# Kernel optimization log

Hardware: AMD Instinct MI355X
Metric: run time of the kernel (lower is better)

The kernel has to match this reference:

```python
import jax, jax.numpy as jnp
import numpy as np

B, N, H = 1024, 100, 256
CLIP = 10.0


def setup_inputs() -> dict:
    key = jax.random.key(0)
    ks = jax.random.split(key, 14)
    s = 0.05  # param scale for numerical stability
    return {
        "x": jax.random.uniform(ks[0], (B, N, 2), jnp.float32),
        "encoder_output": jax.random.normal(ks[1], (B, N, H), jnp.float32),
        "W_ih1": jax.random.normal(ks[2], (3 * H, H + 1), jnp.float32) * s,
        "W_hh1": jax.random.normal(ks[3], (3 * H, H), jnp.float32) * s,
        "b_ih1": jax.random.normal(ks[4], (3 * H,), jnp.float32) * s,
        "b_hh1": jax.random.normal(ks[5], (3 * H,), jnp.float32) * s,
        "W_ih2": jax.random.normal(ks[6], (3 * H, H), jnp.float32) * s,
        "W_hh2": jax.random.normal(ks[7], (3 * H, H), jnp.float32) * s,
        "b_ih2": jax.random.normal(ks[8], (3 * H,), jnp.float32) * s,
        "b_hh2": jax.random.normal(ks[9], (3 * H,), jnp.float32) * s,
        "W_q": jax.random.normal(ks[10], (H, H), jnp.float32) * s,
        "W_ref": jax.random.normal(ks[11], (H, H), jnp.float32) * s,
        "v": jax.random.normal(ks[12], (H,), jnp.float32) * s,
    }


def gru_cell(x, h, W_ih, W_hh, b_ih, b_hh):
    # Standard torch GRU cell math (gate order r, z, n).
    gi = x @ W_ih.T + b_ih
    gh = h @ W_hh.T + b_hh
    i_r, i_z, i_n = jnp.split(gi, 3, axis=-1)
    h_r, h_z, h_n = jnp.split(gh, 3, axis=-1)
    r = jax.nn.sigmoid(i_r + h_r)
    z = jax.nn.sigmoid(i_z + h_z)
    n = jnp.tanh(i_n + r * h_n)
    return (1.0 - z) * n + z * h


def reference(x, encoder_output, W_ih1, W_hh1, b_ih1, b_hh1,
              W_ih2, W_hh2, b_ih2, b_hh2, W_q, W_ref, v):
    Bs, Nn, Hh = encoder_output.shape
    dt = encoder_output.dtype
    # Pointer reference projection is step-invariant -> hoist out of the loop.
    ref = jnp.einsum('bnh,hk->bnk', encoder_output, W_ref)  # [B,N,H]
    bidx = jnp.arange(Bs)
    mask0 = jnp.zeros((Bs, Nn), bool)
    # t=1 context: graph embedding + full remaining capacity D=1.
    ctx0 = jnp.concatenate([encoder_output.mean(1), jnp.ones((Bs, 1), dt)], -1)
    D0 = jnp.ones((Bs,), dt)

    def step(carry, _):
        mask, ctx, D = carry
        z0 = jnp.zeros((Bs, Hh), dt)
        # torch code calls self.gru(last_x) with fresh zero hidden every step
        h1 = gru_cell(ctx, z0, W_ih1, W_hh1, b_ih1, b_hh1)
        h2 = gru_cell(h1, z0, W_ih2, W_hh2, b_ih2, b_hh2)
        q = h2 @ W_q  # [B,H]
        u = CLIP * jnp.tanh(jnp.einsum('bnh,h->bn', jnp.tanh(q[:, None, :] + ref), v))
        u = jnp.where(mask, -1e9, u)  # masked_fill_(mask, -inf)
        nxt = jnp.argmax(u, axis=-1)  # greedy decode (deterministic baseline)
        logp = jax.nn.log_softmax(u, axis=-1)[bidx, nxt]
        mask = mask | (jnp.arange(Nn)[None, :] == nxt[:, None])
        D = D - 1.0 / Nn
        ctx = jnp.concatenate([encoder_output[bidx, nxt], D[:, None]], -1)
        return (mask, ctx, D), (nxt, logp)

    _, (pi_t, lps) = jax.lax.scan(step, (mask0, ctx0, D0), None, length=Nn)
    pi = pi_t.T  # [B, N] tour
    ll = lps.sum(0)  # [B] log-likelihood of tour
    coords = x[bidx[:, None], pi]  # [B,N,2]
    nxt_coords = jnp.roll(coords, -1, axis=1)
    cost = jnp.sqrt(((coords - nxt_coords) ** 2).sum(-1)).sum(-1)  # closed tour length
    return cost, ll
```

## Files before the change

kernel.cpp:

```cpp
#include <hip/hip_runtime.h>
#include <cstdint>
#include <cmath>

#define BATCH 1024
#define SEQ   100
#define HD    256
#define HD3   768
#define NTHR  512
#define NSRC  101

__device__ __forceinline__ float sigmoidf_(float x) { return 1.0f / (1.0f + expf(-x)); }

__device__ __forceinline__ float gru0(float gr, float gz, float gn, float hr, float hz, float hn) {
    float r = sigmoidf_(gr + hr);
    float z = sigmoidf_(gz + hz);
    float n = tanhf(gn + r * hn);
    return (1.0f - z) * n;
}

__global__ __launch_bounds__(256) void init_mean_kernel(const float* __restrict__ enc,
                                                        float* __restrict__ meanenc) {
    int b = blockIdx.x, tid = threadIdx.x;
    const float* e = enc + (size_t)b * SEQ * HD + tid;
    float s = 0.f;
    for (int n = 0; n < SEQ; ++n) s += e[(size_t)n * HD];
    meanenc[(size_t)b * HD + tid] = s * (1.0f / SEQ);
}

__global__ __launch_bounds__(256) void prep_kernel(const float* __restrict__ W_ih1,
                                                   const float* __restrict__ W_ih2,
                                                   float4* __restrict__ W1p4,
                                                   float4* __restrict__ W2p4,
                                                   float* __restrict__ wl,
                                                   float* __restrict__ biasz) {
    int k = blockIdx.x, t = threadIdx.x;
    W1p4[k * HD + t] = make_float4(W_ih1[(size_t)t * (HD + 1) + k],
                                   W_ih1[(size_t)(t + HD) * (HD + 1) + k],
                                   W_ih1[(size_t)(t + 2 * HD) * (HD + 1) + k], 0.f);
    W2p4[k * HD + t] = make_float4(W_ih2[(size_t)t * HD + k],
                                   W_ih2[(size_t)(t + HD) * HD + k],
                                   W_ih2[(size_t)(t + 2 * HD) * HD + k], 0.f);
    if (k == 0) {
#pragma unroll
        for (int c = 0; c < 3; ++c) wl[c * HD + t] = W_ih1[(size_t)(c * HD + t) * (HD + 1) + HD];
        biasz[t] = 0.f;
    }
}

__global__ __launch_bounds__(256) void gemm_bias_kernel(const float* __restrict__ A, int lda,
                                                        const float* __restrict__ Bm, int ldb,
                                                        const float* __restrict__ bias,
                                                        float* __restrict__ C, int ldc) {
    __shared__ float As[16][68];
    __shared__ float Bs[16][68];
    const int tid = threadIdx.x;
    const int tx = tid & 15, ty = tid >> 4;
    const int mBase = blockIdx.x * 64, nBase = blockIdx.y * 64;
    const int lr = tid >> 2, lc = (tid & 3) << 2;
    const int bkk = tid >> 4, bn4 = (tid & 15) << 2;
    float acc[4][4] = {};
    for (int k0 = 0; k0 < HD; k0 += 16) {
        float4 av = *(const float4*)&A[(size_t)(mBase + lr) * lda + k0 + lc];
        As[lc + 0][lr] = av.x; As[lc + 1][lr] = av.y; As[lc + 2][lr] = av.z; As[lc + 3][lr] = av.w;
        float4 bv = *(const float4*)&Bm[(size_t)(k0 + bkk) * ldb + nBase + bn4];
        *(float4*)&Bs[bkk][bn4] = bv;
        __syncthreads();
#pragma unroll
        for (int kk = 0; kk < 16; ++kk) {
            const float4 a4 = *(const float4*)&As[kk][ty << 2];
            const float4 b4 = *(const float4*)&Bs[kk][tx << 2];
            const float ar_[4] = {a4.x, a4.y, a4.z, a4.w};
            const float br_[4] = {b4.x, b4.y, b4.z, b4.w};
#pragma unroll
            for (int i = 0; i < 4; ++i)
#pragma unroll
                for (int j = 0; j < 4; ++j) acc[i][j] = fmaf(ar_[i], br_[j], acc[i][j]);
        }
        __syncthreads();
    }
#pragma unroll
    for (int i = 0; i < 4; ++i) {
        float o[4];
#pragma unroll
        for (int j = 0; j < 4; ++j) o[j] = acc[i][j] + bias[nBase + (tx << 2) + j];
        *(float4*)&C[(size_t)(mBase + (ty << 2) + i) * ldc + nBase + (tx << 2)] =
            make_float4(o[0], o[1], o[2], o[3]);
    }
}

__global__ __launch_bounds__(512) void g1_kernel(const float* __restrict__ enc,
                                                 const float* __restrict__ meanenc,
                                                 const float4* __restrict__ W1p4,
                                                 float* __restrict__ G1) {
    __shared__ float srcs[16][HD];
    __shared__ float part[16][3][HD];
    const int b = blockIdx.x, tid = threadIdx.x;
    const int col = tid & 255, kh = tid >> 8;
    const int kb = kh << 7;
    const float4* wpc = W1p4 + ((size_t)kb << 8) + col;

    for (int nb = 0; nb < 112; nb += 16) {
        for (int e = tid; e < 16 * 64; e += NTHR) {
            const int r = e >> 6, f = e & 63;
            const int n = nb + r;
            float4 vsrc = make_float4(0.f, 0.f, 0.f, 0.f);
            if (n < SEQ)
                vsrc = *(const float4*)&enc[((size_t)b * SEQ + n) * HD + (f << 2)];
            else if (n == SEQ)
                vsrc = *(const float4*)&meanenc[(size_t)b * HD + (f << 2)];
            *(float4*)&srcs[r][f << 2] = vsrc;
        }
        __syncthreads();

        float acc[16][3] = {};
        for (int k = 0; k < 128; k += 8) {
            float4 wv[8];
#pragma unroll
            for (int u = 0; u < 8; ++u) wv[u] = wpc[(size_t)(k + u) << 8];
#pragma unroll
            for (int n = 0; n < 16; ++n) {
#pragma unroll
                for (int uu = 0; uu < 2; ++uu) {
                    const float4 h = *(const float4*)&srcs[n][kb + k + (uu << 2)];
                    const float hv[4] = {h.x, h.y, h.z, h.w};
#pragma unroll
                    for (int u = 0; u < 4; ++u) {
                        const float4 w4 = wv[(uu << 2) + u];
                        acc[n][0] = fmaf(hv[u], w4.x, acc[n][0]);
                        acc[n][1] = fmaf(hv[u], w4.y, acc[n][1]);
                        acc[n][2] = fmaf(hv[u], w4.z, acc[n][2]);
                    }
                }
            }
        }

        if (kh) {
#pragma unroll
            for (int n = 0; n < 16; ++n)
#pragma unroll
                for (int g = 0; g < 3; ++g) part[n][g][col] = acc[n][g];
        }
        __syncthreads();
        if (!kh) {
#pragma unroll
            for (int n = 0; n < 16; ++n) {
                const int nn = nb + n;
                if (nn < NSRC) {
                    float* gp = G1 + ((size_t)(b * NSRC + nn)) * HD3 + col;
                    gp[0]       = acc[n][0] + part[n][0][col];
                    gp[HD]      = acc[n][1] + part[n][1][col];
                    gp[2 * HD]  = acc[n][2] + part[n][2][col];
                }
            }
        }
        __syncthreads();
    }
}

__global__ __launch_bounds__(512, 2) void decode_g1(const float* __restrict__ refb,
                                                    const float* __restrict__ G1,
                                                    const float4* __restrict__ W2p4,
                                                    const float* __restrict__ W_q,
                                                    const float* __restrict__ b_ih1,
                                                    const float* __restrict__ b_hh1,
                                                    const float* __restrict__ b_ih2,
                                                    const float* __restrict__ b_hh2,
                                                    const float* __restrict__ wl,
                                                    const float* __restrict__ vvec,
                                                    const float* __restrict__ x,
                                                    float* __restrict__ out) {
    __shared__ float wls[HD3], bi1s[HD3], bhh1s[HD3], bi2s[HD3], bhh2s[HD3];
    __shared__ float vs[HD];
    __shared__ float h1s[4][HD];
    __shared__ float h2s[4][HD];
    __shared__ float qs[4][HD];
    __shared__ float part[4][3][HD];
    __shared__ float us[4][SEQ];
    __shared__ int   mask_s[4][SEQ];
    __shared__ int   pi_s[4][SEQ];
    __shared__ float ll_s[4];

    const int blk = blockIdx.x, tid = threadIdx.x;
    const int w = tid >> 6, lane = tid & 63;
    const int col = tid & 255, kh = tid >> 8;
    const int b0 = blk << 2;

    for (int j = tid; j < HD3; j += NTHR) {
        wls[j] = wl[j];
        bi1s[j] = b_ih1[j];
        bhh1s[j] = b_hh1[j];
        bi2s[j] = b_ih2[j];
        bhh2s[j] = b_hh2[j];
    }
    if (tid < HD) vs[tid] = vvec[tid];
    if (tid < SEQ) {
#pragma unroll
        for (int bb = 0; bb < 4; ++bb) mask_s[bb][tid] = 0;
    }
    if (tid < 4) ll_s[tid] = 0.f;
    __syncthreads();

    for (int e = tid; e < 4 * HD; e += NTHR) {
        const int bb = e >> 8, c = e & 255;
        const float* gp = G1 + ((size_t)((b0 + bb) * NSRC + SEQ)) * HD3;
        float gr = gp[c] + bi1s[c];                 gr += 1.0f * wls[c];
        float gz = gp[HD + c] + bi1s[c + HD];       gz += 1.0f * wls[c + HD];
        float gn = gp[2 * HD + c] + bi1s[c + 2 * HD]; gn += 1.0f * wls[c + 2 * HD];
        h1s[bb][c] = gru0(gr, gz, gn, bhh1s[c], bhh1s[c + HD], bhh1s[c + 2 * HD]);
    }
    __syncthreads();

    float Dreg = 1.0f;
    const float invN = 1.0f / SEQ;

    auto gru2_phase = [&]() {
        float acc[4][3] = {};
        const int kb = kh << 7;
        const float4* wpc = W2p4 + ((size_t)kb << 8) + col;
        for (int k = 0; k < 128; k += 16) {
            float4 wv[16];
#pragma unroll
            for (int u = 0; u < 16; ++u) wv[u] = wpc[(size_t)(k + u) << 8];
#pragma unroll
            for (int uu = 0; uu < 4; ++uu) {
#pragma unroll
                for (int bb = 0; bb < 4; ++bb) {
                    const float4 h = *(const float4*)&h1s[bb][kb + k + (uu << 2)];
                    const float hv[4] = {h.x, h.y, h.z, h.w};
#pragma unroll
                    for (int u = 0; u < 4; ++u) {
                        const float4 w4 = wv[(uu << 2) + u];
                        acc[bb][0] = fmaf(hv[u], w4.x, acc[bb][0]);
                        acc[bb][1] = fmaf(hv[u], w4.y, acc[bb][1]);
                        acc[bb][2] = fmaf(hv[u], w4.z, acc[bb][2]);
                    }
                }
            }
        }
        if (kh) {
#pragma unroll
            for (int bb = 0; bb < 4; ++bb)
#pragma unroll
                for (int g = 0; g < 3; ++g) part[bb][g][col] = acc[bb][g];
        }
        __syncthreads();
        if (!kh) {
#pragma unroll
            for (int bb = 0; bb < 4; ++bb) {
                float gr = acc[bb][0] + part[bb][0][col] + bi2s[col];
                float gz = acc[bb][1] + part[bb][1][col] + bi2s[col + HD];
                float gn = acc[bb][2] + part[bb][2][col] + bi2s[col + 2 * HD];
                h2s[bb][col] = gru0(gr, gz, gn, bhh2s[col], bhh2s[col + HD], bhh2s[col + 2 * HD]);
            }
        }
    };

    for (int t = 0; t < SEQ; ++t) {
        gru2_phase();
        __syncthreads();
        {
            float qa[4] = {};
            const int kb = kh << 7;
            const float* wqc = W_q + ((size_t)kb << 8) + col;
            for (int k = 0; k < 128; k += 16) {
                float wv[16];
#pragma unroll
                for (int u = 0; u < 16; ++u) wv[u] = wqc[(size_t)(k + u) << 8];
#pragma unroll
                for (int uu = 0; uu < 4; ++uu) {
#pragma unroll
                    for (int bb = 0; bb < 4; ++bb) {
                        const float4 h = *(const float4*)&h2s[bb][kb + k + (uu << 2)];
                        qa[bb] = fmaf(h.x, wv[(uu << 2) + 0], qa[bb]);
                        qa[bb] = fmaf(h.y, wv[(uu << 2) + 1], qa[bb]);
                        qa[bb] = fmaf(h.z, wv[(uu << 2) + 2], qa[bb]);
                        qa[bb] = fmaf(h.w, wv[(uu << 2) + 3], qa[bb]);
                    }
                }
            }
            if (kh) {
#pragma unroll
                for (int bb = 0; bb < 4; ++bb) part[bb][0][col] = qa[bb];
            }
            __syncthreads();
            if (!kh) {
#pragma unroll
                for (int bb = 0; bb < 4; ++bb) qs[bb][col] = qa[bb] + part[bb][0][col];
            }
        }
        __syncthreads();
        {
            const int bq = w & 3;
            const int half = w >> 2;
            const float4 qv = *(const float4*)&qs[bq][lane << 2];
            const float4 vv = *(const float4*)&vs[lane << 2];
            const float* Rb = refb + (size_t)(b0 + bq) * SEQ * HD + (lane << 2);
            const float4 z4 = make_float4(0.f, 0.f, 0.f, 0.f);
            int j = half;
            float4 r0 = *(const float4*)&Rb[(size_t)j * HD];
            float4 r1 = (j + 2 < SEQ) ? *(const float4*)&Rb[(size_t)(j + 2) * HD] : z4;
            float4 r2 = (j + 4 < SEQ) ? *(const float4*)&Rb[(size_t)(j + 4) * HD] : z4;
            float4 r3 = (j + 6 < SEQ) ? *(const float4*)&Rb[(size_t)(j + 6) * HD] : z4;
            while (j < SEQ) {
                float4 rn = z4;
                if (j + 8 < SEQ) rn = *(const float4*)&Rb[(size_t)(j + 8) * HD];
                float s0 = tanhf(qv.x + r0.x) * vv.x;
                s0 = fmaf(tanhf(qv.y + r0.y), vv.y, s0);
                s0 = fmaf(tanhf(qv.z + r0.z), vv.z, s0);
                s0 = fmaf(tanhf(qv.w + r0.w), vv.w, s0);
#pragma unroll
                for (int o = 1; o < 64; o <<= 1) s0 += __shfl_xor(s0, o, 64);
                if (lane == 0) us[bq][j] = 10.0f * tanhf(s0);
                r0 = r1; r1 = r2; r2 = r3; r3 = rn;
                j += 2;
            }
        }
        __syncthreads();
        if (w < 4) {
            const int b = b0 + w;
            const int m0 = mask_s[w][lane];
            float va = m0 ? -3.0e38f : us[w][lane];
            int ia = lane;
            int m1 = 1;
            if (lane + 64 < SEQ) {
                m1 = mask_s[w][lane + 64];
                if (!m1) {
                    float vb2 = us[w][lane + 64];
                    if (vb2 > va) { va = vb2; ia = lane + 64; }
                }
            }
#pragma unroll
            for (int o = 1; o < 64; o <<= 1) {
                float ov = __shfl_xor(va, o, 64);
                int oi = __shfl_xor(ia, o, 64);
                if (ov > va || (ov == va && oi < ia)) { va = ov; ia = oi; }
            }
            float e = (m0 ? 0.0f : expf(us[w][lane] - va)) +
                      ((lane + 64 < SEQ && !m1) ? expf(us[w][lane + 64] - va) : 0.0f);
#pragma unroll
            for (int o = 1; o < 64; o <<= 1) e += __shfl_xor(e, o, 64);
            const int nsel = ia;
            if (lane == 0) {
                ll_s[w] += -logf(e);
                pi_s[w][t] = nsel;
                mask_s[w][nsel] = 1;
            }
            if (t < SEQ - 1) {
                const float Dn = Dreg - invN;
                const float* gp = G1 + ((size_t)(b * NSRC + nsel)) * HD3;
#pragma unroll
                for (int i = 0; i < 4; ++i) {
                    const int c = lane + (i << 6);
                    float gr = gp[c] + bi1s[c];                   gr += Dn * wls[c];
                    float gz = gp[HD + c] + bi1s[c + HD];         gz += Dn * wls[c + HD];
                    float gn = gp[2 * HD + c] + bi1s[c + 2 * HD]; gn += Dn * wls[c + 2 * HD];
                    h1s[w][c] = gru0(gr, gz, gn, bhh1s[c], bhh1s[c + HD], bhh1s[c + 2 * HD]);
                }
            }
        }
        __syncthreads();
        Dreg -= invN;
    }

    if (w < 4) {
        const int b = b0 + w;
        float d = 0.f;
        for (int e2 = lane; e2 < SEQ; e2 += 64) {
            int p = pi_s[w][e2];
            int pn = pi_s[w][(e2 == SEQ - 1) ? 0 : e2 + 1];
            float xa = x[((size_t)b * SEQ + p) * 2 + 0];
            float ya = x[((size_t)b * SEQ + p) * 2 + 1];
            float xb2 = x[((size_t)b * SEQ + pn) * 2 + 0];
            float yb2 = x[((size_t)b * SEQ + pn) * 2 + 1];
            float dx = xa - xb2, dy = ya - yb2;
            d += sqrtf(dx * dx + dy * dy);
        }
#pragma unroll
        for (int o = 1; o < 64; o <<= 1) d += __shfl_xor(d, o, 64);
        if (lane == 0) {
            out[b] = d;
            out[BATCH + b] = ll_s[w];
        }
    }
}

__global__ __launch_bounds__(512, 2) void decode_fallback(const float* __restrict__ refb,
                                                          const float* __restrict__ enc,
                                                          const float* __restrict__ meanenc,
                                                          const float4* __restrict__ W1p4,
                                                          const float4* __restrict__ W2p4,
                                                          const float* __restrict__ W_q,
                                                          const float* __restrict__ b_ih1,
                                                          const float* __restrict__ b_hh1,
                                                          const float* __restrict__ b_ih2,
                                                          const float* __restrict__ b_hh2,
                                                          const float* __restrict__ wl,
                                                          const float* __restrict__ vvec,
                                                          const float* __restrict__ x,
                                                          float* __restrict__ out) {
    __shared__ float wls[HD3], bi1s[HD3], bhh1s[HD3], bi2s[HD3], bhh2s[HD3];
    __shared__ float vs[HD];
    __shared__ float h1s[4][HD];
    __shared__ float h2s[4][HD];
    __shared__ float qs[4][HD];
    __shared__ float encs[4][HD];
    __shared__ float part[4][3][HD];
    __shared__ float us[4][SEQ];
    __shared__ int   rem_s[4][SEQ];
    __shared__ int   pi_s[4][SEQ];
    __shared__ float ll_s[4];

    const int blk = blockIdx.x, tid = threadIdx.x;
    const int w = tid >> 6, lane = tid & 63;
    const int col = tid & 255, kh = tid >> 8;
    const int b0 = blk << 2;

    for (int j = tid; j < HD3; j += NTHR) {
        wls[j] = wl[j];
        bi1s[j] = b_ih1[j];
        bhh1s[j] = b_hh1[j];
        bi2s[j] = b_ih2[j];
        bhh2s[j] = b_hh2[j];
    }
    if (tid < HD) vs[tid] = vvec[tid];
    if (tid < SEQ) {
#pragma unroll
        for (int bb = 0; bb < 4; ++bb) rem_s[bb][tid] = tid;
    }
    if (tid < 4) ll_s[tid] = 0.f;
    for (int e = tid; e < 4 * HD; e += NTHR)
        encs[e >> 8][e & 255] = meanenc[(size_t)(b0 + (e >> 8)) * HD + (e & 255)];
    __syncthreads();

    float Dreg = 1.0f;
    const float invN = 1.0f / SEQ;

    auto gru_phase = [&](const float4* __restrict__ wp, auto& src, auto& dst,
                         const float* __restrict__ bi, const float* __restrict__ bhh,
                         bool useD, float Dv) {
        float acc[4][3] = {};
        const int kb = kh << 7;
        const float4* wpc = wp + ((size_t)kb << 8) + col;
        for (int k = 0; k < 128; k += 16) {
            float4 wv[16];
#pragma unroll
            for (int u = 0; u < 16; ++u) wv[u] = wpc[(size_t)(k + u) << 8];
#pragma unroll
            for (int uu = 0; uu < 4; ++uu) {
#pragma unroll
                for (int bb = 0; bb < 4; ++bb) {
                    const float4 h = *(const float4*)&src[bb][kb + k + (uu << 2)];
                    const float hv[4] = {h.x, h.y, h.z, h.w};
#pragma unroll
                    for (int u = 0; u < 4; ++u) {
                        const float4 w4 = wv[(uu << 2) + u];
                        acc[bb][0] = fmaf(hv[u], w4.x, acc[bb][0]);
                        acc[bb][1] = fmaf(hv[u], w4.y, acc[bb][1]);
                        acc[bb][2] = fmaf(hv[u], w4.z, acc[bb][2]);
                    }
                }
            }
        }
        if (kh) {
#pragma unroll
            for (int bb = 0; bb < 4; ++bb)
#pragma unroll
                for (int g = 0; g < 3; ++g) part[bb][g][col] = acc[bb][g];
        }
        __syncthreads();
        if (!kh) {
#pragma unroll
            for (int bb = 0; bb < 4; ++bb) {
                float gr = acc[bb][0] + part[bb][0][col] + bi[col];
                float gz = acc[bb][1] + part[bb][1][col] + bi[col + HD];
                float gn = acc[bb][2] + part[bb][2][col] + bi[col + 2 * HD];
                if (useD) {
                    gr += Dv * wls[col];
                    gz += Dv * wls[col + HD];
                    gn += Dv * wls[col + 2 * HD];
                }
                dst[bb][col] = gru0(gr, gz, gn, bhh[col], bhh[col + HD], bhh[col + 2 * HD]);
            }
        }
    };

    gru_phase(W1p4, encs, h1s, bi1s, bhh1s, true, Dreg);
    __syncthreads();

    for (int t = 0; t < SEQ; ++t) {
        const int cnt = SEQ - t;
        gru_phase(W2p4, h1s, h2s, bi2s, bhh2s, false, 0.f);
        __syncthreads();
        {
            float qa[4] = {};
            const int kb = kh << 7;
            const float* wqc = W_q + ((size_t)kb << 8) + col;
            for (int k = 0; k < 128; k += 16) {
                float wv[16];
#pragma unroll
                for (int u = 0; u < 16; ++u) wv[u] = wqc[(size_t)(k + u) << 8];
#pragma unroll
                for (int uu = 0; uu < 4; ++uu) {
#pragma unroll
                    for (int bb = 0; bb < 4; ++bb) {
                        const float4 h = *(const float4*)&h2s[bb][kb + k + (uu << 2)];
                        qa[bb] = fmaf(h.x, wv[(uu << 2) + 0], qa[bb]);
                        qa[bb] = fmaf(h.y, wv[(uu << 2) + 1], qa[bb]);
                        qa[bb] = fmaf(h.z, wv[(uu << 2) + 2], qa[bb]);
                        qa[bb] = fmaf(h.w, wv[(uu << 2) + 3], qa[bb]);
                    }
                }
            }
            if (kh) {
#pragma unroll
                for (int bb = 0; bb < 4; ++bb) part[bb][0][col] = qa[bb];
            }
            __syncthreads();
            if (!kh) {
#pragma unroll
                for (int bb = 0; bb < 4; ++bb) qs[bb][col] = qa[bb] + part[bb][0][col];
            }
        }
        __syncthreads();
        {
            const int bq = w & 3;
            const int half = w >> 2;
            const int b = b0 + bq;
            const float4 qv = *(const float4*)&qs[bq][lane << 2];
            const float4 vv = *(const float4*)&vs[lane << 2];
            const float* Rb = refb + (size_t)b * SEQ * HD;
            int j = half;
            float4 rcur = make_float4(0.f, 0.f, 0.f, 0.f);
            if (j < cnt)
                rcur = *(const float4*)&Rb[(size_t)rem_s[bq][j] * HD + (lane << 2)];
            while (j < cnt) {
                const int jn = j + 2;
                float4 rnext = make_float4(0.f, 0.f, 0.f, 0.f);
                if (jn < cnt)
                    rnext = *(const float4*)&Rb[(size_t)rem_s[bq][jn] * HD + (lane << 2)];
                float s0 = tanhf(qv.x + rcur.x) * vv.x;
                s0 = fmaf(tanhf(qv.y + rcur.y), vv.y, s0);
                s0 = fmaf(tanhf(qv.z + rcur.z), vv.z, s0);
                s0 = fmaf(tanhf(qv.w + rcur.w), vv.w, s0);
#pragma unroll
                for (int o = 1; o < 64; o <<= 1) s0 += __shfl_xor(s0, o, 64);
                if (lane == 0) us[bq][j] = 10.0f * tanhf(s0);
                rcur = rnext;
                j = jn;
            }
        }
        __syncthreads();
        if (w < 4) {
            const int b = b0 + w;
            float va = (lane < cnt) ? us[w][lane] : -3.0e38f;
            int ia = lane;
            if (lane + 64 < cnt) {
                float vb2 = us[w][lane + 64];
                if (vb2 > va) { va = vb2; ia = lane + 64; }
            }
#pragma unroll
            for (int o = 1; o < 64; o <<= 1) {
                float ov = __shfl_xor(va, o, 64);
                int oi = __shfl_xor(ia, o, 64);
                if (ov > va || (ov == va && oi < ia)) { va = ov; ia = oi; }
            }
            float e = ((lane < cnt) ? expf(us[w][lane] - va) : 0.0f) +
                      ((lane + 64 < cnt) ? expf(us[w][lane + 64] - va) : 0.0f);
#pragma unroll
            for (int o = 1; o < 64; o <<= 1) e += __shfl_xor(e, o, 64);
            const int nsel = rem_s[w][ia];
            if (lane == 0) {
                ll_s[w] += -logf(e);
                pi_s[w][t] = nsel;
                rem_s[w][ia] = rem_s[w][cnt - 1];
            }
            if (t < SEQ - 1) {
                const float4 ev = *(const float4*)&enc[((size_t)b * SEQ + nsel) * HD + (lane << 2)];
                *(float4*)&encs[w][lane << 2] = ev;
            }
        }
        __syncthreads();
        Dreg -= invN;
        if (t < SEQ - 1) {
            gru_phase(W1p4, encs, h1s, bi1s, bhh1s, true, Dreg);
            __syncthreads();
        }
    }

    if (w < 4) {
        const int b = b0 + w;
        float d = 0.f;
        for (int e2 = lane; e2 < SEQ; e2 += 64) {
            int p = pi_s[w][e2];
            int pn = pi_s[w][(e2 == SEQ - 1) ? 0 : e2 + 1];
            float xa = x[((size_t)b * SEQ + p) * 2 + 0];
            float ya = x[((size_t)b * SEQ + p) * 2 + 1];
            float xb2 = x[((size_t)b * SEQ + pn) * 2 + 0];
            float yb2 = x[((size_t)b * SEQ + pn) * 2 + 1];
            float dx = xa - xb2, dy = ya - yb2;
            d += sqrtf(dx * dx + dy * dy);
        }
#pragma unroll
        for (int o = 1; o < 64; o <<= 1) d += __shfl_xor(d, o, 64);
        if (lane == 0) {
            out[b] = d;
            out[BATCH + b] = ll_s[w];
        }
    }
}

extern "C" void kernel_launch(void* const* d_in, const int* in_sizes, int n_in,
                              void* d_out, int out_size, void* d_ws, size_t ws_size,
                              hipStream_t stream) {
    const float* x     = (const float*)d_in[0];
    const float* enc   = (const float*)d_in[1];
    const float* W_ih1 = (const float*)d_in[2];
    const float* b_ih1 = (const float*)d_in[4];
    const float* b_hh1 = (const float*)d_in[5];
    const float* W_ih2 = (const float*)d_in[6];
    const float* b_ih2 = (const float*)d_in[8];
    const float* b_hh2 = (const float*)d_in[9];
    const float* W_q   = (const float*)d_in[10];
    const float* W_ref = (const float*)d_in[11];
    const float* v     = (const float*)d_in[12];
    float* out = (float*)d_out;
    (void)in_sizes; (void)n_in; (void)out_size;

    char* w = (char*)d_ws;
    size_t off = 0;
    auto take = [&](size_t bytes) {
        char* p = w + off;
        off = (off + bytes + 255) & ~(size_t)255;
        return p;
    };
    float*  refb    = (float*)take((size_t)BATCH * SEQ * HD * 4);
    float*  meanenc = (float*)take((size_t)BATCH * HD * 4);
    float4* W1p4    = (float4*)take((size_t)HD * HD * 16);
    float4* W2p4    = (float4*)take((size_t)HD * HD * 16);
    float*  wl      = (float*)take((size_t)HD3 * 4);
    float*  biasz   = (float*)take((size_t)HD * 4);
    const size_t baseNeed = off;
    float*  G1      = (float*)take((size_t)BATCH * NSRC * HD3 * 4);
    const size_t fullNeed = off;
    if (ws_size < baseNeed) return;
    const bool useG1 = (ws_size >= fullNeed);

    hipLaunchKernelGGL(init_mean_kernel, dim3(BATCH), dim3(HD), 0, stream, enc, meanenc);
    hipLaunchKernelGGL(prep_kernel, dim3(HD), dim3(HD), 0, stream,
                       W_ih1, W_ih2, W1p4, W2p4, wl, biasz);
    hipLaunchKernelGGL(gemm_bias_kernel, dim3(BATCH * SEQ / 64, HD / 64), dim3(256), 0, stream,
                       enc, HD, W_ref, HD, biasz, refb, HD);
    if (useG1) {
        hipLaunchKernelGGL(g1_kernel, dim3(BATCH), dim3(NTHR), 0, stream,
                           enc, meanenc, W1p4, G1);
        hipLaunchKernelGGL(decode_g1, dim3(BATCH / 4), dim3(NTHR), 0, stream,
                           refb, G1, W2p4, W_q,
                           b_ih1, b_hh1, b_ih2, b_hh2, wl, v, x, out);
    } else {
        hipLaunchKernelGGL(decode_fallback, dim3(BATCH / 4), dim3(NTHR), 0, stream,
                           refb, enc, meanenc, W1p4, W2p4, W_q,
                           b_ih1, b_hh1, b_ih2, b_hh2, wl, v, x, out);
    }
}
```

Measured before the change: 5.468 ms.

## Compact remaining-node list in decode and split G1 into batch passes

The decode loop now keeps a per-batch list of unvisited nodes (swap-remove on selection) instead of a mask. Attention scores and tanh are computed only for the remaining nodes, which roughly halves the pointer-attention work over the 100 steps. The host also picks 1, 2 or 4 batch passes so that the precomputed G1 buffer fits in the workspace, using a templated decode with fewer batches per block when more passes are needed. The trade-offs are gathered rather than strided ref loads, extra indirection through the remaining list, and lower per-block batching when more than one pass is used.

```diff
diff --git a/kernel.cpp b/kernel.cpp
--- a/kernel.cpp
+++ b/kernel.cpp
@@ -91,10 +91,12 @@
 __global__ __launch_bounds__(512) void g1_kernel(const float* __restrict__ enc,
                                                  const float* __restrict__ meanenc,
                                                  const float4* __restrict__ W1p4,
-                                                 float* __restrict__ G1) {
+                                                 float* __restrict__ G1,
+                                                 int baseB) {
     __shared__ float srcs[16][HD];
     __shared__ float part[16][3][HD];
-    const int b = blockIdx.x, tid = threadIdx.x;
+    const int bL = blockIdx.x, tid = threadIdx.x;
+    const int gb = baseB + bL;
     const int col = tid & 255, kh = tid >> 8;
     const int kb = kh << 7;
     const float4* wpc = W1p4 + ((size_t)kb << 8) + col;
@@ -105,9 +107,9 @@
             const int n = nb + r;
             float4 vsrc = make_float4(0.f, 0.f, 0.f, 0.f);
             if (n < SEQ)
-                vsrc = *(const float4*)&enc[((size_t)b * SEQ + n) * HD + (f << 2)];
+                vsrc = *(const float4*)&enc[((size_t)gb * SEQ + n) * HD + (f << 2)];
             else if (n == SEQ)
-                vsrc = *(const float4*)&meanenc[(size_t)b * HD + (f << 2)];
+                vsrc = *(const float4*)&meanenc[(size_t)gb * HD + (f << 2)];
             *(float4*)&srcs[r][f << 2] = vsrc;
         }
         __syncthreads();
@@ -146,44 +148,47 @@
             for (int n = 0; n < 16; ++n) {
                 const int nn = nb + n;
                 if (nn < NSRC) {
-                    float* gp = G1 + ((size_t)(b * NSRC + nn)) * HD3 + col;
-                    gp[0]       = acc[n][0] + part[n][0][col];
-                    gp[HD]      = acc[n][1] + part[n][1][col];
-                    gp[2 * HD]  = acc[n][2] + part[n][2][col];
-                }
-            }
-        }
-        __syncthreads();
-    }
-}
-
-__global__ __launch_bounds__(512, 2) void decode_g1(const float* __restrict__ refb,
-                                                    const float* __restrict__ G1,
-                                                    const float4* __restrict__ W2p4,
-                                                    const float* __restrict__ W_q,
-                                                    const float* __restrict__ b_ih1,
-                                                    const float* __restrict__ b_hh1,
-                                                    const float* __restrict__ b_ih2,
-                                                    const float* __restrict__ b_hh2,
-                                                    const float* __restrict__ wl,
-                                                    const float* __restrict__ vvec,
-                                                    const float* __restrict__ x,
-                                                    float* __restrict__ out) {
+                    float* gp = G1 + ((size_t)bL * NSRC + nn) * HD3 + col;
+                    gp[0]      = acc[n][0] + part[n][0][col];
+                    gp[HD]     = acc[n][1] + part[n][1][col];
+                    gp[2 * HD] = acc[n][2] + part[n][2][col];
+                }
+            }
+        }
+        __syncthreads();
+    }
+}
+
+template <int BPB>
+__global__ __launch_bounds__(512, 2) void decode_g1_t(const float* __restrict__ refb,
+                                                      const float* __restrict__ G1,
+                                                      const float4* __restrict__ W2p4,
+                                                      const float* __restrict__ W_q,
+                                                      const float* __restrict__ b_ih1,
+                                                      const float* __restrict__ b_hh1,
+                                                      const float* __restrict__ b_ih2,
+                                                      const float* __restrict__ b_hh2,
+                                                      const float* __restrict__ wl,
+                                                      const float* __restrict__ vvec,
+                                                      const float* __restrict__ x,
+                                                      float* __restrict__ out,
+                                                      int baseB) {
     __shared__ float wls[HD3], bi1s[HD3], bhh1s[HD3], bi2s[HD3], bhh2s[HD3];
     __shared__ float vs[HD];
-    __shared__ float h1s[4][HD];
-    __shared__ float h2s[4][HD];
-    __shared__ float qs[4][HD];
-    __shared__ float part[4][3][HD];
-    __shared__ float us[4][SEQ];
-    __shared__ int   mask_s[4][SEQ];
-    __shared__ int   pi_s[4][SEQ];
-    __shared__ float ll_s[4];
+    __shared__ float h1s[BPB][HD];
+    __shared__ float h2s[BPB][HD];
+    __shared__ float qs[BPB][HD];
+    __shared__ float part[BPB][3][HD];
+    __shared__ float us[BPB][SEQ];
+    __shared__ int   rem_s[BPB][SEQ];
+    __shared__ int   pi_s[BPB][SEQ];
+    __shared__ float ll_s[BPB];
 
     const int blk = blockIdx.x, tid = threadIdx.x;
     const int w = tid >> 6, lane = tid & 63;
     const int col = tid & 255, kh = tid >> 8;
-    const int b0 = blk << 2;
+    const int b0L = blk * BPB;
+    const int b0G = baseB + b0L;
 
     for (int j = tid; j < HD3; j += NTHR) {
         wls[j] = wl[j];
@@ -195,16 +200,16 @@
     if (tid < HD) vs[tid] = vvec[tid];
     if (tid < SEQ) {
 #pragma unroll
-        for (int bb = 0; bb < 4; ++bb) mask_s[bb][tid] = 0;
-    }
-    if (tid < 4) ll_s[tid] = 0.f;
+        for (int bb = 0; bb < BPB; ++bb) rem_s[bb][tid] = tid;
+    }
+    if (tid < BPB) ll_s[tid] = 0.f;
     __syncthreads();
 
-    for (int e = tid; e < 4 * HD; e += NTHR) {
+    for (int e = tid; e < BPB * HD; e += NTHR) {
         const int bb = e >> 8, c = e & 255;
-        const float* gp = G1 + ((size_t)((b0 + bb) * NSRC + SEQ)) * HD3;
-        float gr = gp[c] + bi1s[c];                 gr += 1.0f * wls[c];
-        float gz = gp[HD + c] + bi1s[c + HD];       gz += 1.0f * wls[c + HD];
+        const float* gp = G1 + ((size_t)(b0L + bb) * NSRC + SEQ) * HD3;
+        float gr = gp[c] + bi1s[c];                   gr += 1.0f * wls[c];
+        float gz = gp[HD + c] + bi1s[c + HD];         gz += 1.0f * wls[c + HD];
         float gn = gp[2 * HD + c] + bi1s[c + 2 * HD]; gn += 1.0f * wls[c + 2 * HD];
         h1s[bb][c] = gru0(gr, gz, gn, bhh1s[c], bhh1s[c + HD], bhh1s[c + 2 * HD]);
     }
@@ -213,53 +218,52 @@
     float Dreg = 1.0f;
     const float invN = 1.0f / SEQ;
 
-    auto gru2_phase = [&]() {
-        float acc[4][3] = {};
-        const int kb = kh << 7;
-        const float4* wpc = W2p4 + ((size_t)kb << 8) + col;
-        for (int k = 0; k < 128; k += 16) {
-            float4 wv[16];
-#pragma unroll
-            for (int u = 0; u < 16; ++u) wv[u] = wpc[(size_t)(k + u) << 8];
-#pragma unroll
-            for (int uu = 0; uu < 4; ++uu) {
-#pragma unroll
-                for (int bb = 0; bb < 4; ++bb) {
-                    const float4 h = *(const float4*)&h1s[bb][kb + k + (uu << 2)];
-                    const float hv[4] = {h.x, h.y, h.z, h.w};
-#pragma unroll
-                    for (int u = 0; u < 4; ++u) {
-                        const float4 w4 = wv[(uu << 2) + u];
-                        acc[bb][0] = fmaf(hv[u], w4.x, acc[bb][0]);
-                        acc[bb][1] = fmaf(hv[u], w4.y, acc[bb][1]);
-                        acc[bb][2] = fmaf(hv[u], w4.z, acc[bb][2]);
+    for (int t = 0; t < SEQ; ++t) {
+        const int cnt = SEQ - t;
+        {
+            float acc[BPB][3] = {};
+            const int kb = kh << 7;
+            const float4* wpc = W2p4 + ((size_t)kb << 8) + col;
+            for (int k = 0; k < 128; k += 16) {
+                float4 wv[16];
+#pragma unroll
+                for (int u = 0; u < 16; ++u) wv[u] = wpc[(size_t)(k + u) << 8];
+#pragma unroll
+                for (int uu = 0; uu < 4; ++uu) {
+#pragma unroll
+                    for (int bb = 0; bb < BPB; ++bb) {
+                        const float4 h = *(const float4*)&h1s[bb][kb + k + (uu << 2)];
+                        const float hv[4] = {h.x, h.y, h.z, h.w};
+#pragma unroll
+                        for (int u = 0; u < 4; ++u) {
+                            const float4 w4 = wv[(uu << 2) + u];
+                            acc[bb][0] = fmaf(hv[u], w4.x, acc[bb][0]);
+                            acc[bb][1] = fmaf(hv[u], w4.y, acc[bb][1]);
+                            acc[bb][2] = fmaf(hv[u], w4.z, acc[bb][2]);
+                        }
                     }
                 }
             }
-        }
-        if (kh) {
-#pragma unroll
-            for (int bb = 0; bb < 4; ++bb)
-#pragma unroll
-                for (int g = 0; g < 3; ++g) part[bb][g][col] = acc[bb][g];
-        }
-        __syncthreads();
-        if (!kh) {
-#pragma unroll
-            for (int bb = 0; bb < 4; ++bb) {
-                float gr = acc[bb][0] + part[bb][0][col] + bi2s[col];
-                float gz = acc[bb][1] + part[bb][1][col] + bi2s[col + HD];
-                float gn = acc[bb][2] + part[bb][2][col] + bi2s[col + 2 * HD];
-                h2s[bb][col] = gru0(gr, gz, gn, bhh2s[col], bhh2s[col + HD], bhh2s[col + 2 * HD]);
-            }
-        }
-    };
-
-    for (int t = 0; t < SEQ; ++t) {
-        gru2_phase();
+            if (kh) {
+#pragma unroll
+                for (int bb = 0; bb < BPB; ++bb)
+#pragma unroll
+                    for (int g = 0; g < 3; ++g) part[bb][g][col] = acc[bb][g];
+            }
+            __syncthreads();
+            if (!kh) {
+#pragma unroll
+                for (int bb = 0; bb < BPB; ++bb) {
+                    float gr = acc[bb][0] + part[bb][0][col] + bi2s[col];
+                    float gz = acc[bb][1] + part[bb][1][col] + bi2s[col + HD];
+                    float gn = acc[bb][2] + part[bb][2][col] + bi2s[col + 2 * HD];
+                    h2s[bb][col] = gru0(gr, gz, gn, bhh2s[col], bhh2s[col + HD], bhh2s[col + 2 * HD]);
+                }
+            }
+        }
         __syncthreads();
         {
-            float qa[4] = {};
+            float qa[BPB] = {};
             const int kb = kh << 7;
             const float* wqc = W_q + ((size_t)kb << 8) + col;
             for (int k = 0; k < 128; k += 16) {
@@ -269,7 +273,7 @@
 #pragma unroll
                 for (int uu = 0; uu < 4; ++uu) {
 #pragma unroll
-                    for (int bb = 0; bb < 4; ++bb) {
+                    for (int bb = 0; bb < BPB; ++bb) {
                         const float4 h = *(const float4*)&h2s[bb][kb + k + (uu << 2)];
                         qa[bb] = fmaf(h.x, wv[(uu << 2) + 0], qa[bb]);
                         qa[bb] = fmaf(h.y, wv[(uu << 2) + 1], qa[bb]);
@@ -280,54 +284,50 @@
             }
             if (kh) {
 #pragma unroll
-                for (int bb = 0; bb < 4; ++bb) part[bb][0][col] = qa[bb];
+                for (int bb = 0; bb < BPB; ++bb) part[bb][0][col] = qa[bb];
             }
             __syncthreads();
             if (!kh) {
 #pragma unroll
-                for (int bb = 0; bb < 4; ++bb) qs[bb][col] = qa[bb] + part[bb][0][col];
+                for (int bb = 0; bb < BPB; ++bb) qs[bb][col] = qa[bb] + part[bb][0][col];
             }
         }
         __syncthreads();
         {
-            const int bq = w & 3;
-            const int half = w >> 2;
+            const int bq = w % BPB;
+            const int par = w / BPB;
+            const int str = 8 / BPB;
+            const int bG = b0G + bq;
             const float4 qv = *(const float4*)&qs[bq][lane << 2];
             const float4 vv = *(const float4*)&vs[lane << 2];
-            const float* Rb = refb + (size_t)(b0 + bq) * SEQ * HD + (lane << 2);
-            const float4 z4 = make_float4(0.f, 0.f, 0.f, 0.f);
-            int j = half;
-            float4 r0 = *(const float4*)&Rb[(size_t)j * HD];
-            float4 r1 = (j + 2 < SEQ) ? *(const float4*)&Rb[(size_t)(j + 2) * HD] : z4;
-            float4 r2 = (j + 4 < SEQ) ? *(const float4*)&Rb[(size_t)(j + 4) * HD] : z4;
-            float4 r3 = (j + 6 < SEQ) ? *(const float4*)&Rb[(size_t)(j + 6) * HD] : z4;
-            while (j < SEQ) {
-                float4 rn = z4;
-                if (j + 8 < SEQ) rn = *(const float4*)&Rb[(size_t)(j + 8) * HD];
-                float s0 = tanhf(qv.x + r0.x) * vv.x;
-                s0 = fmaf(tanhf(qv.y + r0.y), vv.y, s0);
-                s0 = fmaf(tanhf(qv.z + r0.z), vv.z, s0);
-                s0 = fmaf(tanhf(qv.w + r0.w), vv.w, s0);
+            const float* Rb = refb + (size_t)bG * SEQ * HD;
+            int j = par;
+            float4 rcur = make_float4(0.f, 0.f, 0.f, 0.f);
+            if (j < cnt)
+                rcur = *(const float4*)&Rb[(size_t)rem_s[bq][j] * HD + (lane << 2)];
+            while (j < cnt) {
+                const int jn = j + str;
+                float4 rnext = make_float4(0.f, 0.f, 0.f, 0.f);
+                if (jn < cnt)
+                    rnext = *(const float4*)&Rb[(size_t)rem_s[bq][jn] * HD + (lane << 2)];
+                float s0 = tanhf(qv.x + rcur.x) * vv.x;
+                s0 = fmaf(tanhf(qv.y + rcur.y), vv.y, s0);
+                s0 = fmaf(tanhf(qv.z + rcur.z), vv.z, s0);
+                s0 = fmaf(tanhf(qv.w + rcur.w), vv.w, s0);
 #pragma unroll
                 for (int o = 1; o < 64; o <<= 1) s0 += __shfl_xor(s0, o, 64);
                 if (lane == 0) us[bq][j] = 10.0f * tanhf(s0);
-                r0 = r1; r1 = r2; r2 = r3; r3 = rn;
-                j += 2;
-            }
-        }
-        __syncthreads();
-        if (w < 4) {
-            const int b = b0 + w;
-            const int m0 = mask_s[w][lane];
-            float va = m0 ? -3.0e38f : us[w][lane];
+                rcur = rnext;
+                j = jn;
+            }
+        }
+        __syncthreads();
+        if (w < BPB) {
+            float va = (lane < cnt) ? us[w][lane] : -3.0e38f;
             int ia = lane;
-            int m1 = 1;
-            if (lane + 64 < SEQ) {
-                m1 = mask_s[w][lane + 64];
-                if (!m1) {
-                    float vb2 = us[w][lane + 64];
-                    if (vb2 > va) { va = vb2; ia = lane + 64; }
-                }
+            if (lane + 64 < cnt) {
+                float vb2 = us[w][lane + 64];
+                if (vb2 > va) { va = vb2; ia = lane + 64; }
             }
 #pragma unroll
             for (int o = 1; o < 64; o <<= 1) {
@@ -335,19 +335,19 @@
                 int oi = __shfl_xor(ia, o, 64);
                 if (ov > va || (ov == va && oi < ia)) { va = ov; ia = oi; }
             }
-            float e = (m0 ? 0.0f : expf(us[w][lane] - va)) +
-                      ((lane + 64 < SEQ && !m1) ? expf(us[w][lane + 64] - va) : 0.0f);
+            float e = ((lane < cnt) ? expf(us[w][lane] - va) : 0.0f) +
+                      ((lane + 64 < cnt) ? expf(us[w][lane + 64] - va) : 0.0f);
 #pragma unroll
             for (int o = 1; o < 64; o <<= 1) e += __shfl_xor(e, o, 64);
-            const int nsel = ia;
+            const int nsel = rem_s[w][ia];
             if (lane == 0) {
                 ll_s[w] += -logf(e);
                 pi_s[w][t] = nsel;
-                mask_s[w][nsel] = 1;
+                rem_s[w][ia] = rem_s[w][cnt - 1];
             }
             if (t < SEQ - 1) {
                 const float Dn = Dreg - invN;
-                const float* gp = G1 + ((size_t)(b * NSRC + nsel)) * HD3;
+                const float* gp = G1 + ((size_t)(b0L + w) * NSRC + nsel) * HD3;
 #pragma unroll
                 for (int i = 0; i < 4; ++i) {
                     const int c = lane + (i << 6);
@@ -362,24 +362,24 @@
         Dreg -= invN;
     }
 
-    if (w < 4) {
-        const int b = b0 + w;
+    if (w < BPB) {
+        const int bG = b0G + w;
         float d = 0.f;
         for (int e2 = lane; e2 < SEQ; e2 += 64) {
             int p = pi_s[w][e2];
             int pn = pi_s[w][(e2 == SEQ - 1) ? 0 : e2 + 1];
-            float xa = x[((size_t)b * SEQ + p) * 2 + 0];
-            float ya = x[((size_t)b * SEQ + p) * 2 + 1];
-            float xb2 = x[((size_t)b * SEQ + pn) * 2 + 0];
-            float yb2 = x[((size_t)b * SEQ + pn) * 2 + 1];
+            float xa = x[((size_t)bG * SEQ + p) * 2 + 0];
+            float ya = x[((size_t)bG * SEQ + p) * 2 + 1];
+            float xb2 = x[((size_t)bG * SEQ + pn) * 2 + 0];
+            float yb2 = x[((size_t)bG * SEQ + pn) * 2 + 1];
             float dx = xa - xb2, dy = ya - yb2;
             d += sqrtf(dx * dx + dy * dy);
         }
 #pragma unroll
         for (int o = 1; o < 64; o <<= 1) d += __shfl_xor(d, o, 64);
         if (lane == 0) {
-            out[b] = d;
-            out[BATCH + b] = ll_s[w];
+            out[bG] = d;
+            out[BATCH + bG] = ll_s[w];
         }
     }
 }
@@ -640,25 +640,47 @@
     float*  wl      = (float*)take((size_t)HD3 * 4);
     float*  biasz   = (float*)take((size_t)HD * 4);
     const size_t baseNeed = off;
-    float*  G1      = (float*)take((size_t)BATCH * NSRC * HD3 * 4);
-    const size_t fullNeed = off;
     if (ws_size < baseNeed) return;
-    const bool useG1 = (ws_size >= fullNeed);
+    const size_t remain = ws_size - baseNeed;
+
+    int npass = 0;
+    for (int np = 1; np <= 4; np <<= 1) {
+        const size_t sb = (size_t)BATCH / np;
+        const size_t g1b = ((sb * NSRC * HD3 * 4) + 255 + 256) & ~(size_t)255;
+        if (g1b <= remain) { npass = np; break; }
+    }
 
     hipLaunchKernelGGL(init_mean_kernel, dim3(BATCH), dim3(HD), 0, stream, enc, meanenc);
     hipLaunchKernelGGL(prep_kernel, dim3(HD), dim3(HD), 0, stream,
                        W_ih1, W_ih2, W1p4, W2p4, wl, biasz);
     hipLaunchKernelGGL(gemm_bias_kernel, dim3(BATCH * SEQ / 64, HD / 64), dim3(256), 0, stream,
                        enc, HD, W_ref, HD, biasz, refb, HD);
-    if (useG1) {
-        hipLaunchKernelGGL(g1_kernel, dim3(BATCH), dim3(NTHR), 0, stream,
-                           enc, meanenc, W1p4, G1);
-        hipLaunchKernelGGL(decode_g1, dim3(BATCH / 4), dim3(NTHR), 0, stream,
-                           refb, G1, W2p4, W_q,
-                           b_ih1, b_hh1, b_ih2, b_hh2, wl, v, x, out);
-    } else {
+
+    if (npass == 0) {
         hipLaunchKernelGGL(decode_fallback, dim3(BATCH / 4), dim3(NTHR), 0, stream,
                            refb, enc, meanenc, W1p4, W2p4, W_q,
                            b_ih1, b_hh1, b_ih2, b_hh2, wl, v, x, out);
-    }
-}
+        return;
+    }
+
+    const int sliceB = BATCH / npass;
+    float* G1 = (float*)take((size_t)sliceB * NSRC * HD3 * 4);
+    for (int pass = 0; pass < npass; ++pass) {
+        const int baseB = pass * sliceB;
+        hipLaunchKernelGGL(g1_kernel, dim3(sliceB), dim3(NTHR), 0, stream,
+                           enc, meanenc, W1p4, G1, baseB);
+        if (npass == 1) {
+            hipLaunchKernelGGL(HIP_KERNEL_NAME(decode_g1_t<4>), dim3(256), dim3(NTHR), 0, stream,
+                               refb, G1, W2p4, W_q, b_ih1, b_hh1, b_ih2, b_hh2,
+                               wl, v, x, out, baseB);
+        } else if (npass == 2) {
+            hipLaunchKernelGGL(HIP_KERNEL_NAME(decode_g1_t<2>), dim3(256), dim3(NTHR), 0, stream,
+                               refb, G1, W2p4, W_q, b_ih1, b_hh1, b_ih2, b_hh2,
+                               wl, v, x, out, baseB);
+        } else {
+            hipLaunchKernelGGL(HIP_KERNEL_NAME(decode_g1_t<1>), dim3(256), dim3(NTHR), 0, stream,
+                               refb, G1, W2p4, W_q, b_ih1, b_hh1, b_ih2, b_hh2,
+                               wl, v, x, out, baseB);
+        }
+    }
+}
```

Measured after the change: 14.02 ms. 2.56x slower.
